# Performance work log

Hardware: AMD Instinct MI355X
Metric: run time of the kernel (lower is better)

Reference implementation:

```python
import jax, jax.numpy as jnp
import numpy as np

EPS = 1e-6
K = 3
R_MIN, R_MAX = 0.5, 2.0


def setup_inputs() -> dict:
    key = jax.random.key(0)
    k0, k1, k2, k3 = jax.random.split(key, 4)
    N, C, D, H, W = 2, 32, 48, 48, 48
    T = 1 + K + 3 + 1  # num_tokens = 6
    x = jax.random.normal(k0, (N, C, D, H, W), jnp.float32)
    w_field = jax.random.normal(k1, (4 * K, C), jnp.float32) * 0.05
    b_field = jnp.zeros((4 * K,), jnp.float32)
    gates = jax.random.normal(k2, (T,), jnp.float32)
    w_mix = jax.random.normal(k3, (C, T * C), jnp.float32) * 0.02
    b_mix = jnp.zeros((C,), jnp.float32)
    return {"x": x, "w_field": w_field, "b_field": b_field, "gates": gates, "w_mix": w_mix, "b_mix": b_mix}


def _reflect(coord, size):
    # torch 'reflection' padding, align_corners=False: reflect over [-0.5, size-0.5]
    c = jnp.abs(coord + 0.5)
    m = jnp.mod(c, 2.0 * size)
    return jnp.minimum(m, 2.0 * size - m) - 0.5


def _trilinear_sample(vol, gx, gy, gz):
    # vol: (N, D, H, W, C) channels-last; gx/gy/gz: (N, K, D, H, W) normalized coords in [-1, 1]
    N, D, H, W, C = vol.shape

    def unnorm(g, size):
        return _reflect(((g + 1.0) * size - 1.0) * 0.5, float(size))

    ix, iy, iz = unnorm(gx, W), unnorm(gy, H), unnorm(gz, D)
    x0 = jnp.floor(ix); y0 = jnp.floor(iy); z0 = jnp.floor(iz)
    fx = (ix - x0)[..., None]; fy = (iy - y0)[..., None]; fz = (iz - z0)[..., None]
    x0i = jnp.clip(x0.astype(jnp.int32), 0, W - 1); x1i = jnp.clip(x0i + 1, 0, W - 1)
    y0i = jnp.clip(y0.astype(jnp.int32), 0, H - 1); y1i = jnp.clip(y0i + 1, 0, H - 1)
    z0i = jnp.clip(z0.astype(jnp.int32), 0, D - 1); z1i = jnp.clip(z0i + 1, 0, D - 1)
    n = jnp.arange(N).reshape(N, 1, 1, 1, 1)

    def g(zi, yi, xi):
        return vol[n, zi, yi, xi]  # (N, K, D, H, W, C)

    c00 = g(z0i, y0i, x0i) * (1.0 - fx) + g(z0i, y0i, x1i) * fx
    c01 = g(z0i, y1i, x0i) * (1.0 - fx) + g(z0i, y1i, x1i) * fx
    c10 = g(z1i, y0i, x0i) * (1.0 - fx) + g(z1i, y0i, x1i) * fx
    c11 = g(z1i, y1i, x0i) * (1.0 - fx) + g(z1i, y1i, x1i) * fx
    c0 = c00 * (1.0 - fy) + c01 * fy
    c1 = c10 * (1.0 - fy) + c11 * fy
    return c0 * (1.0 - fz) + c1 * fz


def reference(x, w_field, b_field, gates, w_mix, b_mix):
    N, C, D, H, W = x.shape
    # field head: 1x1x1 conv C -> 4K, split into K unit directions U and radii r
    f = jnp.einsum('ncdhw,oc->nodhw', x, w_field) + b_field[None, :, None, None, None]
    f = f.reshape(N, K, 4, D, H, W)
    v = f[:, :, :3]
    U = v / jnp.sqrt(jnp.sum(v * v, axis=2, keepdims=True) + EPS)  # (N,K,3,D,H,W)
    r_s = R_MIN + (R_MAX - R_MIN) * jax.nn.sigmoid(f[:, :, 3])     # (N,K,D,H,W)
    # base grid, align_corners=False normalized coordinates
    gz0 = ((jnp.arange(D, dtype=x.dtype) + 0.5) * 2.0 / D - 1.0)[:, None, None]
    gy0 = ((jnp.arange(H, dtype=x.dtype) + 0.5) * 2.0 / H - 1.0)[None, :, None]
    gx0 = ((jnp.arange(W, dtype=x.dtype) + 0.5) * 2.0 / W - 1.0)[None, None, :]
    ux, uy, uz = U[:, :, 0], U[:, :, 1], U[:, :, 2]
    dx = 2.0 * r_s * ux / (W + EPS)
    dy = 2.0 * r_s * uy / (H + EPS)
    dz = 2.0 * r_s * uz / (D + EPS)
    vol = jnp.transpose(x, (0, 2, 3, 4, 1))  # (N,D,H,W,C)
    xp = _trilinear_sample(vol, gx0 + dx, gy0 + dy, gz0 + dz)  # (N,K,D,H,W,C)
    xm = _trilinear_sample(vol, gx0 - dx, gy0 - dy, gz0 - dz)
    xp = jnp.transpose(xp, (0, 1, 5, 2, 3, 4))  # (N,K,C,D,H,W)
    xm = jnp.transpose(xm, (0, 1, 5, 2, 3, 4))
    a = 0.5 * (xp + xm)
    o = 0.5 * (xp - xm)
    inv_r = 1.0 / (jax.lax.stop_gradient(r_s) + EPS)  # r detached in original
    d1 = o * inv_r[:, :, None]                        # (N,K,C,D,H,W)
    G = jnp.einsum('nkadhw,nkcdhw->nacdhw', U, d1)     # (N,3,C,D,H,W)
    d2 = (xp + xm - 2.0 * x[:, None]) * (inv_r * inv_r)[:, :, None]
    L = d2.mean(axis=1)                                # (N,C,D,H,W)
    tokens = jnp.concatenate([x[:, None], a, G, L[:, None]], axis=1)  # (N,T,C,D,H,W)
    T = tokens.shape[1]
    gated = tokens * jax.nn.sigmoid(gates)[None, :, None, None, None, None]
    delta = jnp.einsum('nmdhw,om->nodhw', gated.reshape(N, T * C, D, H, W), w_mix)
    delta = delta + b_mix[None, :, None, None, None]
    return x + delta
```

## Files before the change

kernel.cpp:

```cpp
#include <hip/hip_runtime.h>
#include <math.h>

#define NB   2
#define CH   32
#define DHW  (48*48*48)
#define TT   8
#define EPSF 1e-6f

#define TILE_N   1521
#define TILE_WSTR 1522
#define TILE_BYTES (TILE_WSTR*16)
#define GROUPS   4

#define TOK_OFF  0
#define TOK_STR  64
#define TILE_OFF 16384
#define SMEM_SZ  (16384 + 2*TILE_BYTES)

#define WS_BT_F 0
#define WS_WF   4096
#define WS_BF   4480
#define WS_BM   4492

typedef __attribute__((ext_vector_type(8))) short short8;
typedef __attribute__((ext_vector_type(8))) _Float16 half8;
typedef __attribute__((ext_vector_type(4))) float floatx4;
typedef __attribute__((ext_vector_type(2))) _Float16 h2;

struct __align__(16) q8v { h2 q[4]; };

__device__ __forceinline__ h2 pkrtz(float a, float b) {
    return __builtin_bit_cast(h2, __builtin_amdgcn_cvt_pkrtz(a, b));
}
__device__ __forceinline__ unsigned pkrtz_u(float a, float b) {
    return __builtin_bit_cast(unsigned, __builtin_amdgcn_cvt_pkrtz(a, b));
}
__device__ __forceinline__ q8v ldq8(const char* p) {
    return __builtin_bit_cast(q8v, *(const half8*)p);
}
__device__ __forceinline__ void stq8(char* p, q8v v) {
    *(half8*)p = __builtin_bit_cast(half8, v);
}

__global__ __launch_bounds__(256) void prep_kernel(
        const float* __restrict__ w_field,
        const float* __restrict__ b_field,
        const float* __restrict__ gates,
        const float* __restrict__ w_mix,
        const float* __restrict__ b_mix,
        float* __restrict__ ws) {
    int i = blockIdx.x * 256 + threadIdx.x;
    {
        int o = i >> 8, k = i & 255, c = k >> 3, t = k & 7;
        float sg = 1.0f / (1.0f + expf(-gates[t]));
        _Float16 hv = (_Float16)(sg * w_mix[o * 256 + t * 32 + c]);
        ((unsigned short*)(ws + WS_BT_F))[o * 256 + k] = __builtin_bit_cast(unsigned short, hv);
    }
    if (i < 384) { int c = i / 12, o = i - c * 12; ws[WS_WF + i] = w_field[o * 32 + c]; }
    if (i < 12)  ws[WS_BF + i] = b_field[i];
    if (i < 32)  ws[WS_BM + i] = b_mix[i];
}

__global__ __launch_bounds__(256) void geo_main(
        const float* __restrict__ x,
        const float* __restrict__ ws,
        float* __restrict__ out) {
    __shared__ __align__(16) char smem[SMEM_SZ];
    char* tokb  = smem + TOK_OFF;
    char* tileb = smem + TILE_OFF;
    float* cbuf = (float*)smem;

    const int tid = threadIdx.x;
    const int lin = (blockIdx.x & 7) * 108 + (blockIdx.x >> 3);
    const int bx = lin % 6, by = (lin / 6) % 6, bz = (lin / 36) % 12, n = lin / 432;
    const int lx = tid & 7, ly = (tid >> 3) & 7, lz = tid >> 6;
    const int w = bx * 8 + lx, h = by * 8 + ly, d = bz * 4 + lz;
    const int xlo = bx * 8 - 2, ylo = by * 8 - 2, zlo = bz * 4 - 2;
    const int lane = tid & 63, w64 = tid & 192;

    const float* xn = x + (size_t)n * CH * DHW;

    int goff[6];
#pragma unroll
    for (int i = 0; i < 6; ++i) {
        int e  = tid + i * 256;
        int ee = (e < TILE_N) ? e : 0;
        int tz = ee / 169; int r0 = ee - tz * 169;
        int ty = r0 / 13;  int tx = r0 - ty * 13;
        int zg = min(max(zlo + tz, 0), 47);
        int yg = min(max(ylo + ty, 0), 47);
        int xg = min(max(xlo + tx, 0), 47);
        goff[i] = (zg * 48 + yg) * 48 + xg;
    }

    const int pos = (d * 48 + h) * 48 + w;
    float f[12];
#pragma unroll
    for (int o = 0; o < 12; ++o) f[o] = ws[WS_BF + o];
    for (int c = 0; c < CH; ++c) {
        float xv = xn[c * DHW + pos];
        const float* wf = ws + WS_WF + c * 12;
#pragma unroll
        for (int o = 0; o < 12; ++o) f[o] = fmaf(wf[o], xv, f[o]);
    }

    h2 fx2[6], fy2[6], fz2[6];
    int a00[6], a01[6], a10[6], a11[6];
    float uxk[3], uyk[3], uzk[3], irk[3], ir2k[3];
    const float cscale = 48.0f / (48.0f + EPSF);
#pragma unroll
    for (int k = 0; k < 3; ++k) {
        float vx = f[4*k], vy = f[4*k+1], vz = f[4*k+2], s = f[4*k+3];
        float inv = 1.0f / sqrtf(vx*vx + vy*vy + vz*vz + EPSF);
        float ux = vx * inv, uy = vy * inv, uz = vz * inv;
        float r  = 0.5f + 1.5f / (1.0f + expf(-s));
        uxk[k] = ux; uyk[k] = uy; uzk[k] = uz;
        float ir = 1.0f / (r + EPSF); irk[k] = ir; ir2k[k] = ir * ir;
#pragma unroll
        for (int sgn = 0; sgn < 2; ++sgn) {
            int   si = 2 * k + sgn;
            float sf = sgn ? -1.0f : 1.0f;
            float txr = (float)w + sf * r * ux * cscale;
            float tyr = (float)h + sf * r * uy * cscale;
            float tzr = (float)d + sf * r * uz * cscale;
            float cx = fabsf(txr + 0.5f); float ix = fminf(cx, 96.0f - cx) - 0.5f;
            float cy = fabsf(tyr + 0.5f); float iy = fminf(cy, 96.0f - cy) - 0.5f;
            float cz = fabsf(tzr + 0.5f); float iz = fminf(cz, 96.0f - cz) - 0.5f;
            float x0f = floorf(ix), y0f = floorf(iy), z0f = floorf(iz);
            float fx = ix - x0f, fy = iy - y0f, fz = iz - z0f;
            int x0 = min(max((int)x0f, 0), 47); int x1 = min(x0 + 1, 47);
            int y0 = min(max((int)y0f, 0), 47); int y1 = min(y0 + 1, 47);
            int z0 = min(max((int)z0f, 0), 47); int z1 = min(z0 + 1, 47);
            float fxe = (x1 == x0) ? 0.0f : fx;
            _Float16 hx = (_Float16)fxe, hy = (_Float16)fy, hz = (_Float16)fz;
            fx2[si] = (h2){hx, hx}; fy2[si] = (h2){hy, hy}; fz2[si] = (h2){hz, hz};
            int lz0 = z0 - zlo, lz1 = z1 - zlo;
            int ly0 = y0 - ylo, ly1 = y1 - ylo;
            int lx0 = x0 - xlo;
            a00[si] = (lz0 * 13 + ly0) * 13 + lx0;
            a01[si] = (lz0 * 13 + ly1) * 13 + lx0;
            a10[si] = (lz1 * 13 + ly0) * 13 + lx0;
            a11[si] = (lz1 * 13 + ly1) * 13 + lx0;
        }
    }

    if (tid == 0) {
        q8v z; z.q[0] = (h2){0,0}; z.q[1] = (h2){0,0}; z.q[2] = (h2){0,0}; z.q[3] = (h2){0,0};
        stq8(tileb + TILE_N * 16, z);
        stq8(tileb + TILE_BYTES + TILE_N * 16, z);
    }
    {
        float ld[48];
#pragma unroll
        for (int cg = 0; cg < 8; ++cg) {
            const float* xc = xn + cg * DHW;
#pragma unroll
            for (int i = 0; i < 6; ++i) ld[cg * 6 + i] = xc[goff[i]];
        }
#pragma unroll
        for (int i = 0; i < 6; ++i) {
            int e = tid + i * 256;
            if (e < TILE_N) {
                q8v vq;
                vq.q[0] = pkrtz(ld[i],      ld[6  + i]);
                vq.q[1] = pkrtz(ld[12 + i], ld[18 + i]);
                vq.q[2] = pkrtz(ld[24 + i], ld[30 + i]);
                vq.q[3] = pkrtz(ld[36 + i], ld[42 + i]);
                stq8(tileb + e * 16, vq);
            }
        }
    }

    q8v pqv[6];
    {
        float l2[48];
#pragma unroll
        for (int cg = 0; cg < 8; ++cg) {
            const float* xc = xn + (8 + cg) * DHW;
#pragma unroll
            for (int i = 0; i < 6; ++i) l2[cg * 6 + i] = xc[goff[i]];
        }
#pragma unroll
        for (int i = 0; i < 6; ++i) {
            pqv[i].q[0] = pkrtz(l2[i],      l2[6  + i]);
            pqv[i].q[1] = pkrtz(l2[12 + i], l2[18 + i]);
            pqv[i].q[2] = pkrtz(l2[24 + i], l2[30 + i]);
            pqv[i].q[3] = pkrtz(l2[36 + i], l2[42 + i]);
        }
    }
    __syncthreads();

    floatx4 acc[4][2];
#pragma unroll
    for (int mt = 0; mt < 4; ++mt)
#pragma unroll
        for (int nt = 0; nt < 2; ++nt) acc[mt][nt] = (floatx4){0.f, 0.f, 0.f, 0.f};

    const int self = ((lz + 2) * 13 + (ly + 2)) * 13 + (lx + 2);
    const unsigned short* bt = (const unsigned short*)(ws + WS_BT_F);
    const int tokq = (tid >> 3) & 3;
    const int qm = lane >> 4, nlo = lane & 15;

    short8 bcA0 = *(const short8*)(bt + (nlo * 256 + 0 * 32 + qm * 8));
    short8 bcA1 = *(const short8*)(bt + ((nlo + 16) * 256 + 0 * 32 + qm * 8));
    short8 bcB0 = *(const short8*)(bt + (nlo * 256 + 1 * 32 + qm * 8));
    short8 bcB1 = *(const short8*)(bt + ((nlo + 16) * 256 + 1 * 32 + qm * 8));

    for (int g = 0; g < GROUPS; ++g) {
        const int rb = (g & 1);
        const int wb = rb ^ 1;
        if (g < GROUPS - 1) {
#pragma unroll
            for (int i = 0; i < 6; ++i) {
                int e = tid + i * 256;
                if (e < TILE_N) stq8(tileb + wb * TILE_BYTES + e * 16, pqv[i]);
            }
        }
        float nld[48];
        if (g < GROUPS - 2) {
            const float* xg = xn + (g + 2) * 8 * DHW;
#pragma unroll
            for (int cg = 0; cg < 8; ++cg) {
                const float* xc = xg + cg * DHW;
#pragma unroll
                for (int i = 0; i < 6; ++i) nld[cg * 6 + i] = xc[goff[i]];
            }
        }
        short8 bnA0 = bcA0, bnA1 = bcA1, bnB0 = bcB0, bnB1 = bcB1;
        if (g < GROUPS - 1) {
            int cc = 2 * (g + 1);
            bnA0 = *(const short8*)(bt + (nlo * 256 + cc * 32 + qm * 8));
            bnA1 = *(const short8*)(bt + ((nlo + 16) * 256 + cc * 32 + qm * 8));
            bnB0 = *(const short8*)(bt + (nlo * 256 + (cc + 1) * 32 + qm * 8));
            bnB1 = *(const short8*)(bt + ((nlo + 16) * 256 + (cc + 1) * 32 + qm * 8));
        }
        const char* tb = tileb + rb * TILE_BYTES;
        q8v s2 = ldq8(tb + self * 16);
        q8v vv[6];
#pragma unroll
        for (int si = 0; si < 6; ++si) {
            int b00 = a00[si], b01 = a01[si], b10 = a10[si], b11 = a11[si];
            q8v v000 = ldq8(tb + b00 * 16), v001 = ldq8(tb + b00 * 16 + 16);
            q8v v010 = ldq8(tb + b01 * 16), v011 = ldq8(tb + b01 * 16 + 16);
            q8v v100 = ldq8(tb + b10 * 16), v101 = ldq8(tb + b10 * 16 + 16);
            q8v v110 = ldq8(tb + b11 * 16), v111 = ldq8(tb + b11 * 16 + 16);
            h2 fx = fx2[si], fy = fy2[si], fz = fz2[si];
#pragma unroll
            for (int qd = 0; qd < 4; ++qd) {
                h2 c00 = v000.q[qd] + fx * (v001.q[qd] - v000.q[qd]);
                h2 c01 = v010.q[qd] + fx * (v011.q[qd] - v010.q[qd]);
                h2 c10 = v100.q[qd] + fx * (v101.q[qd] - v100.q[qd]);
                h2 c11 = v110.q[qd] + fx * (v111.q[qd] - v110.q[qd]);
                h2 c0  = c00 + fy * (c01 - c00);
                h2 c1  = c10 + fy * (c11 - c10);
                vv[si].q[qd] = c0 + fz * (c1 - c0);
            }
        }
#pragma unroll
        for (int p = 0; p < 2; ++p) {
#pragma unroll
            for (int j = 0; j < 4; ++j) {
                const int ce = p * 4 + j;
                float xv = (ce & 1) ? (float)s2.q[ce >> 1].y : (float)s2.q[ce >> 1].x;
                float val[6];
#pragma unroll
                for (int si = 0; si < 6; ++si)
                    val[si] = (ce & 1) ? (float)vv[si].q[ce >> 1].y : (float)vv[si].q[ce >> 1].x;
                float t1, t2, t3, gx, gy, gz, l;
                {
                    float sp, sm, d1;
                    sp = val[0]; sm = val[1]; t1 = 0.5f * (sp + sm);
                    d1 = 0.5f * (sp - sm) * irk[0];
                    gx = uxk[0] * d1; gy = uyk[0] * d1; gz = uzk[0] * d1;
                    l  = (sp + sm - 2.0f * xv) * ir2k[0];
                    sp = val[2]; sm = val[3]; t2 = 0.5f * (sp + sm);
                    d1 = 0.5f * (sp - sm) * irk[1];
                    gx = fmaf(uxk[1], d1, gx); gy = fmaf(uyk[1], d1, gy); gz = fmaf(uzk[1], d1, gz);
                    l  = fmaf(sp + sm - 2.0f * xv, ir2k[1], l);
                    sp = val[4]; sm = val[5]; t3 = 0.5f * (sp + sm);
                    d1 = 0.5f * (sp - sm) * irk[2];
                    gx = fmaf(uxk[2], d1, gx); gy = fmaf(uyk[2], d1, gy); gz = fmaf(uzk[2], d1, gz);
                    l  = fmaf(sp + sm - 2.0f * xv, ir2k[2], l);
                }
                uint4 tw;
                tw.x = pkrtz_u(xv, t1);
                tw.y = pkrtz_u(t2, t3);
                tw.z = pkrtz_u(gx, gy);
                tw.w = pkrtz_u(gz, l * (1.0f / 3.0f));
                int qe = j ^ tokq;
                *(uint4*)(tokb + tid * TOK_STR + qe * 16) = tw;
            }
            {
                short8 b0 = p ? bcB0 : bcA0;
                short8 b1 = p ? bcB1 : bcA1;
                half8 hb0 = __builtin_bit_cast(half8, b0);
                half8 hb1 = __builtin_bit_cast(half8, b1);
#pragma unroll
                for (int mt = 0; mt < 4; ++mt) {
                    int row = w64 + mt * 16 + nlo;
                    int qe  = qm ^ ((row >> 3) & 3);
                    half8 a = __builtin_bit_cast(half8,
                              *(const short8*)(tokb + row * TOK_STR + qe * 16));
                    acc[mt][0] = __builtin_amdgcn_mfma_f32_16x16x32_f16(a, hb0, acc[mt][0], 0, 0, 0);
                    acc[mt][1] = __builtin_amdgcn_mfma_f32_16x16x32_f16(a, hb1, acc[mt][1], 0, 0, 0);
                }
            }
        }
        bcA0 = bnA0; bcA1 = bnA1; bcB0 = bnB0; bcB1 = bnB1;

        if (g < GROUPS - 2) {
#pragma unroll
            for (int i = 0; i < 6; ++i) {
                pqv[i].q[0] = pkrtz(nld[i],      nld[6  + i]);
                pqv[i].q[1] = pkrtz(nld[12 + i], nld[18 + i]);
                pqv[i].q[2] = pkrtz(nld[24 + i], nld[30 + i]);
                pqv[i].q[3] = pkrtz(nld[36 + i], nld[42 + i]);
            }
        }
        __syncthreads();
    }

    {
#pragma unroll
        for (int mt = 0; mt < 4; ++mt)
#pragma unroll
            for (int nt = 0; nt < 2; ++nt)
#pragma unroll
                for (int r = 0; r < 4; ++r) {
                    int vr = w64 + mt * 16 + qm * 4 + r;
                    int col = nt * 16 + nlo;
                    cbuf[vr * 36 + (col ^ (vr & 31))] = acc[mt][nt][r];
                }
    }
    __syncthreads();

    const float* dr = cbuf + tid * 36;
    float* on = out + (size_t)n * CH * DHW;
#pragma unroll
    for (int o = 0; o < 32; ++o)
        __builtin_nontemporal_store(
            xn[o * DHW + pos] + dr[o ^ (tid & 31)] + ws[WS_BM + o],
            on + o * DHW + pos);
}

extern "C" void kernel_launch(void* const* d_in, const int* in_sizes, int n_in,
                              void* d_out, int out_size, void* d_ws, size_t ws_size,
                              hipStream_t stream) {
    const float *x = (const float*)d_in[0], *w_field = (const float*)d_in[1],
                *b_field = (const float*)d_in[2], *gates = (const float*)d_in[3],
                *w_mix = (const float*)d_in[4], *b_mix = (const float*)d_in[5];
    for (int i = 0; i < n_in; ++i) {
        switch (in_sizes[i]) {
            case NB * CH * DHW: x       = (const float*)d_in[i]; break;
            case 12 * CH:       w_field = (const float*)d_in[i]; break;
            case 12:            b_field = (const float*)d_in[i]; break;
            case TT:            gates   = (const float*)d_in[i]; break;
            case CH * TT * CH:  w_mix   = (const float*)d_in[i]; break;
            case CH:            b_mix   = (const float*)d_in[i]; break;
            default: break;
        }
    }
    float* ws = (float*)d_ws;
    prep_kernel<<<32, 256, 0, stream>>>(w_field, b_field, gates, w_mix, b_mix, ws);
    geo_main<<<864, 256, 0, stream>>>(x, ws, (float*)d_out);
}
```

Baseline: 179.2 us.

## Single-buffer the LDS halo tile and split channel-group prefetch to cut registers

Replaces the double-buffered LDS tile with a single buffer, which roughly halves the tile's shared memory. The next channel group's global loads are split into two halves issued at different points in the loop, and the register-resident packed prefetch and cached B-fragments are dropped. B-fragments are now reloaded from global inside the MFMA step. The aim is lower register and LDS pressure so more blocks fit per CU. The cost is an extra barrier per group and less overlap between tile writes and compute.

```diff
diff --git a/kernel.cpp b/kernel.cpp
--- a/kernel.cpp
+++ b/kernel.cpp
@@ -15,7 +15,7 @@
 #define TOK_OFF  0
 #define TOK_STR  64
 #define TILE_OFF 16384
-#define SMEM_SZ  (16384 + 2*TILE_BYTES)
+#define SMEM_SZ  (16384 + TILE_BYTES)
 
 #define WS_BT_F 0
 #define WS_WF   4096
@@ -147,7 +147,6 @@
     if (tid == 0) {
         q8v z; z.q[0] = (h2){0,0}; z.q[1] = (h2){0,0}; z.q[2] = (h2){0,0}; z.q[3] = (h2){0,0};
         stq8(tileb + TILE_N * 16, z);
-        stq8(tileb + TILE_BYTES + TILE_N * 16, z);
     }
     {
         float ld[48];
@@ -170,24 +169,6 @@
             }
         }
     }
-
-    q8v pqv[6];
-    {
-        float l2[48];
-#pragma unroll
-        for (int cg = 0; cg < 8; ++cg) {
-            const float* xc = xn + (8 + cg) * DHW;
-#pragma unroll
-            for (int i = 0; i < 6; ++i) l2[cg * 6 + i] = xc[goff[i]];
-        }
-#pragma unroll
-        for (int i = 0; i < 6; ++i) {
-            pqv[i].q[0] = pkrtz(l2[i],      l2[6  + i]);
-            pqv[i].q[1] = pkrtz(l2[12 + i], l2[18 + i]);
-            pqv[i].q[2] = pkrtz(l2[24 + i], l2[30 + i]);
-            pqv[i].q[3] = pkrtz(l2[36 + i], l2[42 + i]);
-        }
-    }
     __syncthreads();
 
     floatx4 acc[4][2];
@@ -201,40 +182,18 @@
     const int tokq = (tid >> 3) & 3;
     const int qm = lane >> 4, nlo = lane & 15;
 
-    short8 bcA0 = *(const short8*)(bt + (nlo * 256 + 0 * 32 + qm * 8));
-    short8 bcA1 = *(const short8*)(bt + ((nlo + 16) * 256 + 0 * 32 + qm * 8));
-    short8 bcB0 = *(const short8*)(bt + (nlo * 256 + 1 * 32 + qm * 8));
-    short8 bcB1 = *(const short8*)(bt + ((nlo + 16) * 256 + 1 * 32 + qm * 8));
-
     for (int g = 0; g < GROUPS; ++g) {
-        const int rb = (g & 1);
-        const int wb = rb ^ 1;
+        float nldA[24];
         if (g < GROUPS - 1) {
-#pragma unroll
-            for (int i = 0; i < 6; ++i) {
-                int e = tid + i * 256;
-                if (e < TILE_N) stq8(tileb + wb * TILE_BYTES + e * 16, pqv[i]);
-            }
-        }
-        float nld[48];
-        if (g < GROUPS - 2) {
-            const float* xg = xn + (g + 2) * 8 * DHW;
-#pragma unroll
-            for (int cg = 0; cg < 8; ++cg) {
+            const float* xg = xn + (g + 1) * 8 * DHW;
+#pragma unroll
+            for (int cg = 0; cg < 4; ++cg) {
                 const float* xc = xg + cg * DHW;
 #pragma unroll
-                for (int i = 0; i < 6; ++i) nld[cg * 6 + i] = xc[goff[i]];
-            }
-        }
-        short8 bnA0 = bcA0, bnA1 = bcA1, bnB0 = bcB0, bnB1 = bcB1;
-        if (g < GROUPS - 1) {
-            int cc = 2 * (g + 1);
-            bnA0 = *(const short8*)(bt + (nlo * 256 + cc * 32 + qm * 8));
-            bnA1 = *(const short8*)(bt + ((nlo + 16) * 256 + cc * 32 + qm * 8));
-            bnB0 = *(const short8*)(bt + (nlo * 256 + (cc + 1) * 32 + qm * 8));
-            bnB1 = *(const short8*)(bt + ((nlo + 16) * 256 + (cc + 1) * 32 + qm * 8));
-        }
-        const char* tb = tileb + rb * TILE_BYTES;
+                for (int i = 0; i < 6; ++i) nldA[cg * 6 + i] = xc[goff[i]];
+            }
+        }
+        const char* tb = tileb;
         q8v s2 = ldq8(tb + self * 16);
         q8v vv[6];
 #pragma unroll
@@ -254,6 +213,22 @@
                 h2 c0  = c00 + fy * (c01 - c00);
                 h2 c1  = c10 + fy * (c11 - c10);
                 vv[si].q[qd] = c0 + fz * (c1 - c0);
+            }
+        }
+        h2 pqA[12];
+        float nldB[24];
+        if (g < GROUPS - 1) {
+#pragma unroll
+            for (int i = 0; i < 6; ++i) {
+                pqA[i]     = pkrtz(nldA[i],      nldA[6  + i]);
+                pqA[6 + i] = pkrtz(nldA[12 + i], nldA[18 + i]);
+            }
+            const float* xg = xn + ((g + 1) * 8 + 4) * DHW;
+#pragma unroll
+            for (int cg = 0; cg < 4; ++cg) {
+                const float* xc = xg + cg * DHW;
+#pragma unroll
+                for (int i = 0; i < 6; ++i) nldB[cg * 6 + i] = xc[goff[i]];
             }
         }
 #pragma unroll
@@ -291,10 +266,11 @@
                 *(uint4*)(tokb + tid * TOK_STR + qe * 16) = tw;
             }
             {
-                short8 b0 = p ? bcB0 : bcA0;
-                short8 b1 = p ? bcB1 : bcA1;
-                half8 hb0 = __builtin_bit_cast(half8, b0);
-                half8 hb1 = __builtin_bit_cast(half8, b1);
+                const int cc = 2 * g + p;
+                half8 hb0 = __builtin_bit_cast(half8,
+                            *(const short8*)(bt + (nlo * 256 + cc * 32 + qm * 8)));
+                half8 hb1 = __builtin_bit_cast(half8,
+                            *(const short8*)(bt + ((nlo + 16) * 256 + cc * 32 + qm * 8)));
 #pragma unroll
                 for (int mt = 0; mt < 4; ++mt) {
                     int row = w64 + mt * 16 + nlo;
@@ -306,15 +282,20 @@
                 }
             }
         }
-        bcA0 = bnA0; bcA1 = bnA1; bcB0 = bnB0; bcB1 = bnB1;
-
-        if (g < GROUPS - 2) {
+        __syncthreads();
+
+        if (g < GROUPS - 1) {
 #pragma unroll
             for (int i = 0; i < 6; ++i) {
-                pqv[i].q[0] = pkrtz(nld[i],      nld[6  + i]);
-                pqv[i].q[1] = pkrtz(nld[12 + i], nld[18 + i]);
-                pqv[i].q[2] = pkrtz(nld[24 + i], nld[30 + i]);
-                pqv[i].q[3] = pkrtz(nld[36 + i], nld[42 + i]);
+                int e = tid + i * 256;
+                if (e < TILE_N) {
+                    q8v vq;
+                    vq.q[0] = pqA[i];
+                    vq.q[1] = pqA[6 + i];
+                    vq.q[2] = pkrtz(nldB[i],      nldB[6  + i]);
+                    vq.q[3] = pkrtz(nldB[12 + i], nldB[18 + i]);
+                    stq8(tileb + e * 16, vq);
+                }
             }
         }
         __syncthreads();
```

Result: no change. 179.9 us (+0.4%).
